# Kernel tuning notes

Hardware: AMD Instinct MI355X
Metric: run time of the kernel (lower is better)

Reference implementation:

```python
import jax, jax.numpy as jnp
import numpy as np

IN0, OUT0 = 64, 64   # layer 0: input_size -> hidden
IN1, OUT1 = 64, 16   # layer 1: hidden -> output_size
H = 2                # subnetwork hidden width (subnetwork_shape=[2,2])
BATCH = 16384


def _make_layer_params(key, n_subnets):
    ks = jax.random.split(key, 6)
    s1 = 1.0  # fan_in=1
    s2 = 1.0 / np.sqrt(H)
    W1 = jax.random.uniform(ks[0], (n_subnets, H, 1), minval=-s1, maxval=s1)
    b1 = jax.random.uniform(ks[1], (n_subnets, H), minval=-s1, maxval=s1)
    W2 = jax.random.uniform(ks[2], (n_subnets, H, H), minval=-s2, maxval=s2)
    b2 = jax.random.uniform(ks[3], (n_subnets, H), minval=-s2, maxval=s2)
    W3 = jax.random.uniform(ks[4], (n_subnets, 1, H), minval=-s2, maxval=s2)
    b3 = jax.random.uniform(ks[5], (n_subnets, 1), minval=-s2, maxval=s2)
    return W1, b1, W2, b2, W3, b3


def setup_inputs() -> dict:
    key = jax.random.key(0)
    kx, k0, k1 = jax.random.split(key, 3)
    x = jax.random.normal(kx, (BATCH, IN0), dtype=jnp.float32)
    l0 = _make_layer_params(k0, IN0 * OUT0)
    l1 = _make_layer_params(k1, IN1 * OUT1)
    names = ['W1', 'b1', 'W2', 'b2', 'W3', 'b3']
    inp = {'x': x}
    for n, v in zip(names, l0):
        inp['l0_' + n] = v
    for n, v in zip(names, l1):
        inp['l1_' + n] = v
    return inp


def _kan_layer(x, in_size, out_size, W1, b1, W2, b2, W3, b3):
    # x: [B, in] -> x_expanded: [in*out, B, 1]; subnet n = i*out + o
    B = x.shape[0]
    xe = jnp.repeat(x.T, out_size, axis=0)[:, :, None]          # [N, B, 1]
    h = jax.nn.relu(jnp.einsum('nbi,nhi->nbh', xe, W1) + b1[:, None, :])  # [N, B, H]
    h = jax.nn.relu(jnp.einsum('nbh,nkh->nbk', h, W2) + b2[:, None, :])   # [N, B, H]
    o = jnp.einsum('nbk,nok->nbo', h, W3) + b3[:, None, :]                # [N, B, 1]
    o = o[..., 0].reshape(in_size, out_size, B).sum(axis=0)               # [out, B]
    return o.T                                                            # [B, out]


def reference(x, l0_W1, l0_b1, l0_W2, l0_b2, l0_W3, l0_b3,
              l1_W1, l1_b1, l1_W2, l1_b2, l1_W3, l1_b3):
    h = _kan_layer(x, IN0, OUT0, l0_W1, l0_b1, l0_W2, l0_b2, l0_W3, l0_b3)
    out = _kan_layer(h, IN1, OUT1, l1_W1, l1_b1, l1_W2, l1_b2, l1_W3, l1_b3)
    return out
```

## Files before the change

### kernel.cpp

```cpp
#include <hip/hip_runtime.h>


typedef float v2f __attribute__((ext_vector_type(2)));

#define BATCH 16384
#define TB    32

__global__ __launch_bounds__(256, 2) void kan_fused(
    const float* __restrict__ x,
    const float* __restrict__ A1, const float* __restrict__ a1,
    const float* __restrict__ A2, const float* __restrict__ a2,
    const float* __restrict__ A3, const float* __restrict__ a3,
    const float* __restrict__ B1, const float* __restrict__ c1,
    const float* __restrict__ B2, const float* __restrict__ c2,
    const float* __restrict__ B3, const float* __restrict__ c3,
    float* __restrict__ out)
{
    __shared__ float xs[64][36];
    __shared__ float hp[2][TB][64];
    __shared__ float ht[64][36];
    __shared__ float op[2][TB][16];

    const int t    = threadIdx.x;
    const int lane = t & 63;
    const int wave = t >> 6;
    const int ih   = wave & 1;
    const int bh   = wave >> 1;
    const int bB0  = blockIdx.x * TB;

    for (int k = t * 4; k < TB * 64; k += 256 * 4) {
        const float4 v = *(const float4*)(x + (long)bB0 * 64 + k);
        const int b = k >> 6, i = k & 63;
        xs[i][b] = v.x; xs[i + 1][b] = v.y; xs[i + 2][b] = v.z; xs[i + 3][b] = v.w;
    }
    __syncthreads();

    const v2f zz = {0.f, 0.f};

    {
        const int o     = lane;
        const int ibase = 32 * ih;
        const int boff  = 16 * bh;

        auto ldw = [&](int i, v2f& w1, v2f& d1, float4& w2, v2f& d2, v2f& w3, float& b3v) {
            const int n = (i << 6) + o;
            w1  = *(const v2f*)(A1 + 2 * n);
            d1  = *(const v2f*)(a1 + 2 * n);
            w2  = *(const float4*)(A2 + 4 * n);
            d2  = *(const v2f*)(a2 + 2 * n);
            w3  = *(const v2f*)(A3 + 2 * n);
            b3v = a3[n];
        };
        auto ldx = [&](int i, float4* xv) {
            xv[0] = *(const float4*)&xs[i][boff];
            xv[1] = *(const float4*)&xs[i][boff + 4];
            xv[2] = *(const float4*)&xs[i][boff + 8];
            xv[3] = *(const float4*)&xs[i][boff + 12];
        };

        float acc[16];
#pragma unroll
        for (int j = 0; j < 16; ++j) acc[j] = 0.f;
        float bsum = 0.f;

        v2f w1, d1, d2, w3; float4 w2; float b3v;
        float4 xv[4];
        ldw(ibase, w1, d1, w2, d2, w3, b3v);
        ldx(ibase, xv);

#pragma unroll 1
        for (int ii = 0; ii < 32; ++ii) {
            const int inext = ibase + ((ii + 1) & 31);
            v2f nw1, nd1, nd2, nw3; float4 nw2; float nb3;
            float4 xn[4];
            ldw(inext, nw1, nd1, nw2, nd2, nw3, nb3);
            ldx(inext, xn);

            bsum += b3v;
            const v2f c0  = {w2.x, w2.z};
            const v2f c1v = {w2.y, w2.w};
#pragma unroll
            for (int j = 0; j < 16; ++j) {
                const float xb = ((const float*)xv)[j];
                const v2f xd = {xb, xb};
                v2f m = __builtin_elementwise_fma(xd, w1, d1);
                m = __builtin_elementwise_max(m, zz);
                const v2f mm0 = {m.x, m.x};
                const v2f mm1 = {m.y, m.y};
                v2f tt = __builtin_elementwise_fma(c1v, mm1, d2);
                tt = __builtin_elementwise_fma(c0, mm0, tt);
                tt = __builtin_elementwise_max(tt, zz);
                acc[j] = fmaf(w3.x, tt.x, fmaf(w3.y, tt.y, acc[j]));
            }
            w1 = nw1; d1 = nd1; w2 = nw2; d2 = nd2; w3 = nw3; b3v = nb3;
            xv[0] = xn[0]; xv[1] = xn[1]; xv[2] = xn[2]; xv[3] = xn[3];
        }
#pragma unroll
        for (int j = 0; j < 16; ++j)
            hp[ih][boff + j][o] = acc[j] + bsum;
    }
    __syncthreads();

    for (int k = t; k < TB * 64; k += 256) {
        const int b = k >> 6, i = k & 63;
        ht[i][b] = hp[0][b][i] + hp[1][b][i];
    }
    __syncthreads();

    {
        const int o1   = lane & 15;
        const int iq   = lane >> 4;
        const int i0   = 32 * ih + 8 * iq;
        const int boff = 16 * bh;

        auto ldw = [&](int i, v2f& w1, v2f& d1, float4& w2, v2f& d2, v2f& w3, float& b3v) {
            const int n = (i << 4) + o1;
            w1  = *(const v2f*)(B1 + 2 * n);
            d1  = *(const v2f*)(c1 + 2 * n);
            w2  = *(const float4*)(B2 + 4 * n);
            d2  = *(const v2f*)(c2 + 2 * n);
            w3  = *(const v2f*)(B3 + 2 * n);
            b3v = c3[n];
        };
        auto ldh = [&](int i, float4* hv) {
            hv[0] = *(const float4*)&ht[i][boff];
            hv[1] = *(const float4*)&ht[i][boff + 4];
            hv[2] = *(const float4*)&ht[i][boff + 8];
            hv[3] = *(const float4*)&ht[i][boff + 12];
        };

        float acc[16];
#pragma unroll
        for (int j = 0; j < 16; ++j) acc[j] = 0.f;
        float bsum = 0.f;

        v2f w1, d1, d2, w3; float4 w2; float b3v;
        float4 hv[4];
        ldw(i0, w1, d1, w2, d2, w3, b3v);
        ldh(i0, hv);

#pragma unroll 1
        for (int ii = 0; ii < 8; ++ii) {
            const int inext = i0 + ((ii + 1) & 7);
            v2f nw1, nd1, nd2, nw3; float4 nw2; float nb3;
            float4 hn[4];
            ldw(inext, nw1, nd1, nw2, nd2, nw3, nb3);
            ldh(inext, hn);

            bsum += b3v;
            const v2f c0  = {w2.x, w2.z};
            const v2f c1v = {w2.y, w2.w};
#pragma unroll
            for (int j = 0; j < 16; ++j) {
                const float hb = ((const float*)hv)[j];
                const v2f xd = {hb, hb};
                v2f m = __builtin_elementwise_fma(xd, w1, d1);
                m = __builtin_elementwise_max(m, zz);
                const v2f mm0 = {m.x, m.x};
                const v2f mm1 = {m.y, m.y};
                v2f tt = __builtin_elementwise_fma(c1v, mm1, d2);
                tt = __builtin_elementwise_fma(c0, mm0, tt);
                tt = __builtin_elementwise_max(tt, zz);
                acc[j] = fmaf(w3.x, tt.x, fmaf(w3.y, tt.y, acc[j]));
            }
            w1 = nw1; d1 = nd1; w2 = nw2; d2 = nd2; w3 = nw3; b3v = nb3;
            hv[0] = hn[0]; hv[1] = hn[1]; hv[2] = hn[2]; hv[3] = hn[3];
        }

#pragma unroll
        for (int j = 0; j < 16; ++j) {
            float v = acc[j] + bsum;
            v += __shfl_xor(v, 16, 64);
            v += __shfl_xor(v, 32, 64);
            if (iq == 0) op[ih][16 * bh + j][o1] = v;
        }
    }
    __syncthreads();

    if (t < 128) {
        const int f = t * 4;
        const float4 u = *(const float4*)(&op[0][0][0] + f);
        const float4 v = *(const float4*)(&op[1][0][0] + f);
        float4 r;
        r.x = u.x + v.x; r.y = u.y + v.y; r.z = u.z + v.z; r.w = u.w + v.w;
        *(float4*)(out + (long)bB0 * 16 + f) = r;
    }
}

extern "C" void kernel_launch(void* const* d_in, const int* in_sizes, int n_in,
                              void* d_out, int out_size, void* d_ws, size_t ws_size,
                              hipStream_t stream) {
    const float* x     = (const float*)d_in[0];
    const float* l0_W1 = (const float*)d_in[1];
    const float* l0_b1 = (const float*)d_in[2];
    const float* l0_W2 = (const float*)d_in[3];
    const float* l0_b2 = (const float*)d_in[4];
    const float* l0_W3 = (const float*)d_in[5];
    const float* l0_b3 = (const float*)d_in[6];
    const float* l1_W1 = (const float*)d_in[7];
    const float* l1_b1 = (const float*)d_in[8];
    const float* l1_W2 = (const float*)d_in[9];
    const float* l1_b2 = (const float*)d_in[10];
    const float* l1_W3 = (const float*)d_in[11];
    const float* l1_b3 = (const float*)d_in[12];

    float* outp = (float*)d_out;

    dim3 blk(256);
    dim3 grid(BATCH / TB);
    hipLaunchKernelGGL(kan_fused, grid, blk, 0, stream,
                       x,
                       l0_W1, l0_b1, l0_W2, l0_b2, l0_W3, l0_b3,
                       l1_W1, l1_b1, l1_W2, l1_b2, l1_W3, l1_b3,
                       outp);
}
```

Before: 105.5 us.

## Split input dimension across four waves per batch half with 512-thread blocks

Doubles the block to 512 threads and splits the input-feature reduction four ways instead of two, so each wave processes 16 inputs in layer 0 and 4 inputs per lane group in layer 1. Partial sums are combined through larger shared-memory buffers. The x prefetch from LDS moves into the loop body instead of being software-pipelined. This gives more waves per batch tile and more latency hiding, at the cost of extra shared memory, more reduction traffic and a tighter register budget under launch_bounds(512,4).

```diff
diff --git a/kernel.cpp b/kernel.cpp
--- a/kernel.cpp
+++ b/kernel.cpp
@@ -6,7 +6,7 @@
 #define BATCH 16384
 #define TB    32
 
-__global__ __launch_bounds__(256, 2) void kan_fused(
+__global__ __launch_bounds__(512, 4) void kan_fused(
     const float* __restrict__ x,
     const float* __restrict__ A1, const float* __restrict__ a1,
     const float* __restrict__ A2, const float* __restrict__ a2,
@@ -17,18 +17,19 @@
     float* __restrict__ out)
 {
     __shared__ float xs[64][36];
-    __shared__ float hp[2][TB][64];
+    __shared__ float hp[4][TB][64];
     __shared__ float ht[64][36];
-    __shared__ float op[2][TB][16];
+    __shared__ float op[4][TB][16];
 
     const int t    = threadIdx.x;
     const int lane = t & 63;
     const int wave = t >> 6;
-    const int ih   = wave & 1;
-    const int bh   = wave >> 1;
+    const int iq   = wave & 3;
+    const int bh   = wave >> 2;
     const int bB0  = blockIdx.x * TB;
 
-    for (int k = t * 4; k < TB * 64; k += 256 * 4) {
+    {
+        const int k = t * 4;
         const float4 v = *(const float4*)(x + (long)bB0 * 64 + k);
         const int b = k >> 6, i = k & 63;
         xs[i][b] = v.x; xs[i + 1][b] = v.y; xs[i + 2][b] = v.z; xs[i + 3][b] = v.w;
@@ -36,11 +37,11 @@
     __syncthreads();
 
     const v2f zz = {0.f, 0.f};
+    const int boff = 16 * bh;
 
     {
-        const int o     = lane;
-        const int ibase = 32 * ih;
-        const int boff  = 16 * bh;
+        const int o  = lane;
+        const int i0 = 16 * iq;
 
         auto ldw = [&](int i, v2f& w1, v2f& d1, float4& w2, v2f& d2, v2f& w3, float& b3v) {
             const int n = (i << 6) + o;
@@ -51,12 +52,6 @@
             w3  = *(const v2f*)(A3 + 2 * n);
             b3v = a3[n];
         };
-        auto ldx = [&](int i, float4* xv) {
-            xv[0] = *(const float4*)&xs[i][boff];
-            xv[1] = *(const float4*)&xs[i][boff + 4];
-            xv[2] = *(const float4*)&xs[i][boff + 8];
-            xv[3] = *(const float4*)&xs[i][boff + 12];
-        };
 
         float acc[16];
 #pragma unroll
@@ -64,17 +59,19 @@
         float bsum = 0.f;
 
         v2f w1, d1, d2, w3; float4 w2; float b3v;
-        float4 xv[4];
-        ldw(ibase, w1, d1, w2, d2, w3, b3v);
-        ldx(ibase, xv);
+        ldw(i0, w1, d1, w2, d2, w3, b3v);
 
 #pragma unroll 1
-        for (int ii = 0; ii < 32; ++ii) {
-            const int inext = ibase + ((ii + 1) & 31);
+        for (int ii = 0; ii < 16; ++ii) {
+            const int i = i0 + ii;
             v2f nw1, nd1, nd2, nw3; float4 nw2; float nb3;
-            float4 xn[4];
-            ldw(inext, nw1, nd1, nw2, nd2, nw3, nb3);
-            ldx(inext, xn);
+            ldw(i0 + ((ii + 1) & 15), nw1, nd1, nw2, nd2, nw3, nb3);
+
+            const float4 xv0 = *(const float4*)&xs[i][boff];
+            const float4 xv1 = *(const float4*)&xs[i][boff + 4];
+            const float4 xv2 = *(const float4*)&xs[i][boff + 8];
+            const float4 xv3 = *(const float4*)&xs[i][boff + 12];
+            const float4 xv[4] = {xv0, xv1, xv2, xv3};
 
             bsum += b3v;
             const v2f c0  = {w2.x, w2.z};
@@ -93,25 +90,23 @@
                 acc[j] = fmaf(w3.x, tt.x, fmaf(w3.y, tt.y, acc[j]));
             }
             w1 = nw1; d1 = nd1; w2 = nw2; d2 = nd2; w3 = nw3; b3v = nb3;
-            xv[0] = xn[0]; xv[1] = xn[1]; xv[2] = xn[2]; xv[3] = xn[3];
         }
 #pragma unroll
         for (int j = 0; j < 16; ++j)
-            hp[ih][boff + j][o] = acc[j] + bsum;
-    }
-    __syncthreads();
-
-    for (int k = t; k < TB * 64; k += 256) {
+            hp[iq][boff + j][o] = acc[j] + bsum;
+    }
+    __syncthreads();
+
+    for (int k = t; k < TB * 64; k += 512) {
         const int b = k >> 6, i = k & 63;
-        ht[i][b] = hp[0][b][i] + hp[1][b][i];
+        ht[i][b] = hp[0][b][i] + hp[1][b][i] + hp[2][b][i] + hp[3][b][i];
     }
     __syncthreads();
 
     {
-        const int o1   = lane & 15;
-        const int iq   = lane >> 4;
-        const int i0   = 32 * ih + 8 * iq;
-        const int boff = 16 * bh;
+        const int o1 = lane & 15;
+        const int ig = lane >> 4;
+        const int i0 = 16 * iq + 4 * ig;
 
         auto ldw = [&](int i, v2f& w1, v2f& d1, float4& w2, v2f& d2, v2f& w3, float& b3v) {
             const int n = (i << 4) + o1;
@@ -122,12 +117,6 @@
             w3  = *(const v2f*)(B3 + 2 * n);
             b3v = c3[n];
         };
-        auto ldh = [&](int i, float4* hv) {
-            hv[0] = *(const float4*)&ht[i][boff];
-            hv[1] = *(const float4*)&ht[i][boff + 4];
-            hv[2] = *(const float4*)&ht[i][boff + 8];
-            hv[3] = *(const float4*)&ht[i][boff + 12];
-        };
 
         float acc[16];
 #pragma unroll
@@ -135,17 +124,19 @@
         float bsum = 0.f;
 
         v2f w1, d1, d2, w3; float4 w2; float b3v;
-        float4 hv[4];
         ldw(i0, w1, d1, w2, d2, w3, b3v);
-        ldh(i0, hv);
 
 #pragma unroll 1
-        for (int ii = 0; ii < 8; ++ii) {
-            const int inext = i0 + ((ii + 1) & 7);
+        for (int ii = 0; ii < 4; ++ii) {
+            const int i = i0 + ii;
             v2f nw1, nd1, nd2, nw3; float4 nw2; float nb3;
-            float4 hn[4];
-            ldw(inext, nw1, nd1, nw2, nd2, nw3, nb3);
-            ldh(inext, hn);
+            ldw(i0 + ((ii + 1) & 3), nw1, nd1, nw2, nd2, nw3, nb3);
+
+            const float4 hv0 = *(const float4*)&ht[i][boff];
+            const float4 hv1 = *(const float4*)&ht[i][boff + 4];
+            const float4 hv2 = *(const float4*)&ht[i][boff + 8];
+            const float4 hv3 = *(const float4*)&ht[i][boff + 12];
+            const float4 hv[4] = {hv0, hv1, hv2, hv3};
 
             bsum += b3v;
             const v2f c0  = {w2.x, w2.z};
@@ -164,7 +155,6 @@
                 acc[j] = fmaf(w3.x, tt.x, fmaf(w3.y, tt.y, acc[j]));
             }
             w1 = nw1; d1 = nd1; w2 = nw2; d2 = nd2; w3 = nw3; b3v = nb3;
-            hv[0] = hn[0]; hv[1] = hn[1]; hv[2] = hn[2]; hv[3] = hn[3];
         }
 
 #pragma unroll
@@ -172,17 +162,22 @@
             float v = acc[j] + bsum;
             v += __shfl_xor(v, 16, 64);
             v += __shfl_xor(v, 32, 64);
-            if (iq == 0) op[ih][16 * bh + j][o1] = v;
+            if (ig == 0) op[iq][boff + j][o1] = v;
         }
     }
     __syncthreads();
 
     if (t < 128) {
         const int f = t * 4;
-        const float4 u = *(const float4*)(&op[0][0][0] + f);
-        const float4 v = *(const float4*)(&op[1][0][0] + f);
+        const float4 p0 = *(const float4*)(&op[0][0][0] + f);
+        const float4 p1 = *(const float4*)(&op[1][0][0] + f);
+        const float4 p2 = *(const float4*)(&op[2][0][0] + f);
+        const float4 p3 = *(const float4*)(&op[3][0][0] + f);
         float4 r;
-        r.x = u.x + v.x; r.y = u.y + v.y; r.z = u.z + v.z; r.w = u.w + v.w;
+        r.x = p0.x + p1.x + p2.x + p3.x;
+        r.y = p0.y + p1.y + p2.y + p3.y;
+        r.z = p0.z + p1.z + p2.z + p3.z;
+        r.w = p0.w + p1.w + p2.w + p3.w;
         *(float4*)(out + (long)bB0 * 16 + f) = r;
     }
 }
@@ -206,7 +201,7 @@
 
     float* outp = (float*)d_out;
 
-    dim3 blk(256);
+    dim3 blk(512);
     dim3 grid(BATCH / TB);
     hipLaunchKernelGGL(kan_fused, grid, blk, 0, stream,
                        x,
```

After: 102.1 us. 3.2% less time.
